# Kernel tuning notes

Measured on AMD Instinct MI355X. Metric: run time of the kernel, lower is better.

Reference implementation:

```python
import jax, jax.numpy as jnp
import numpy as np

NUM_SELECT = 300

def _cxcywh_to_xyxy(b):
    cx, cy, w, h = b[..., 0], b[..., 1], b[..., 2], b[..., 3]
    return jnp.stack([cx - w * 0.5, cy - h * 0.5, cx + w * 0.5, cy + h * 0.5], axis=-1)

def setup_inputs() -> dict:
    key = jax.random.key(0)
    k1, k2, k3 = jax.random.split(key, 3)
    B, Q, C = 512, 900, 256
    pred_logits = jax.random.normal(k1, (B, Q, C), dtype=jnp.float32)
    pred_boxes = jax.random.uniform(k2, (B, Q, 4), dtype=jnp.float32)  # normalized cxcywh in [0,1)
    target_sizes = jax.random.uniform(k3, (B, 2), dtype=jnp.float32) * 1333.0 + 1.0  # (h, w)
    return {"pred_logits": pred_logits, "pred_boxes": pred_boxes, "target_sizes": target_sizes}

def reference(pred_logits, pred_boxes, target_sizes):
    B, Q, C = pred_logits.shape
    prob = jax.nn.sigmoid(pred_logits)                      # [B,Q,C]
    flat = prob.reshape(B, Q * C)
    topk_vals, topk_idxs = jax.lax.top_k(flat, NUM_SELECT)  # [B,K]
    scores = topk_vals
    topk_boxes = topk_idxs // C                              # query index
    labels = topk_idxs % C                                   # class index
    out_boxes = _cxcywh_to_xyxy(pred_boxes)                  # [B,Q,4]
    out_boxes = jnp.take_along_axis(out_boxes, topk_boxes[:, :, None], axis=1)  # [B,K,4]
    img_h, img_w = target_sizes[:, 0], target_sizes[:, 1]
    scale = jnp.stack([img_w, img_h, img_w, img_h], axis=1)  # [B,4]
    out_boxes = out_boxes * scale[:, None, :]
    return scores, labels, out_boxes
```

## Files before the change

kernel.cpp:

```cpp
#include <hip/hip_runtime.h>
#include <math.h>


#define NB 512
#define NQ 900
#define NC 256
#define NELEM (NQ*NC)
#define NF4 (NELEM/4)
#define NSEL 300
#define NT 1024
#define HBINS 8192
#define CAP 2048

typedef unsigned long long ull;

__device__ __forceinline__ unsigned keyOf(float f) {
    unsigned u = __float_as_uint(f);
    return u ^ ((unsigned)((int)u >> 31) | 0x80000000u);
}
__device__ __forceinline__ float keyToFloat(unsigned k) {
    unsigned u = (k & 0x80000000u) ? (k ^ 0x80000000u) : ~k;
    return __uint_as_float(u);
}

__global__ __launch_bounds__(NT) void detpost_kernel(
    const float* __restrict__ logits, const float* __restrict__ boxes,
    const float* __restrict__ tsizes, float* __restrict__ out)
{
    __shared__ unsigned hist[HBINS];
    __shared__ ull zb[CAP];
    __shared__ unsigned suf[NT];
    __shared__ unsigned sT, sCand, sAbove, sDone, sCnt;

    const int tid = threadIdx.x;
    const int row = blockIdx.x;
    const float4* __restrict__ r4 = (const float4*)(logits + (size_t)row * NELEM);

    unsigned W0 = 0;
    unsigned sh = 19;
    unsigned above = 0;
    unsigned T, cand;

    while (true) {
        for (int i = tid; i < HBINS; i += NT) hist[i] = 0;
        __syncthreads();

        unsigned i0 = tid;
        #pragma unroll 1
        for (int it = 0; it < 14; ++it, i0 += 4096) {
            float4 a = r4[i0];
            float4 b = r4[i0 + 1024];
            float4 c = r4[i0 + 2048];
            float4 d = r4[i0 + 3072];
            #define PH(f) { unsigned k = keyOf(f); unsigned bin = (k - W0) >> sh; \
                            if (bin < HBINS) atomicAdd(&hist[bin], 1u); }
            PH(a.x) PH(a.y) PH(a.z) PH(a.w)
            PH(b.x) PH(b.y) PH(b.z) PH(b.w)
            PH(c.x) PH(c.y) PH(c.z) PH(c.w)
            PH(d.x) PH(d.y) PH(d.z) PH(d.w)
        }
        if (tid < 256) {
            float4 a = r4[57344 + tid];
            PH(a.x) PH(a.y) PH(a.z) PH(a.w)
        }
        __syncthreads();

        unsigned local = 0;
        #pragma unroll
        for (int j = 0; j < 8; ++j) local += hist[tid * 8 + j];
        suf[tid] = local;
        __syncthreads();
        for (int off = 1; off < NT; off <<= 1) {
            unsigned v = suf[tid] + ((tid + off < NT) ? suf[tid + off] : 0u);
            __syncthreads();
            suf[tid] = v;
            __syncthreads();
        }
        unsigned mySuf = suf[tid];
        unsigned nxt = (tid < NT - 1) ? suf[tid + 1] : 0u;
        if (above + mySuf >= NSEL && above + nxt < NSEL) {
            unsigned run = above + nxt;
            for (int j = 7; j >= 0; --j) {
                unsigned h = hist[tid * 8 + j];
                run += h;
                if (run >= NSEL) {
                    sT = W0 + ((unsigned)(tid * 8 + j) << sh);
                    sCand = run;
                    sAbove = run - h;
                    sDone = (run <= CAP || sh == 0) ? 1u : 0u;
                    break;
                }
            }
        }
        __syncthreads();
        T = sT; cand = sCand;
        if (sDone) break;
        above = sAbove;
        W0 = T;
        sh = (sh >= 13) ? (sh - 13) : 0u;
        __syncthreads();
    }
    (void)cand;

    if (tid == 0) sCnt = 0;
    __syncthreads();
    {
        unsigned i0 = tid;
        #pragma unroll 1
        for (int it = 0; it < 14; ++it, i0 += 4096) {
            float4 a = r4[i0];
            float4 b = r4[i0 + 1024];
            float4 c = r4[i0 + 2048];
            float4 d = r4[i0 + 3072];
            #define PC(f, ei) { unsigned k = keyOf(f); if (k >= T) { \
                unsigned p = atomicAdd(&sCnt, 1u); \
                if (p < CAP) zb[p] = ((ull)k << 32) | (unsigned)~(unsigned)(ei); } }
            PC(a.x, i0*4+0)          PC(a.y, i0*4+1)          PC(a.z, i0*4+2)          PC(a.w, i0*4+3)
            PC(b.x, (i0+1024)*4+0)   PC(b.y, (i0+1024)*4+1)   PC(b.z, (i0+1024)*4+2)   PC(b.w, (i0+1024)*4+3)
            PC(c.x, (i0+2048)*4+0)   PC(c.y, (i0+2048)*4+1)   PC(c.z, (i0+2048)*4+2)   PC(c.w, (i0+2048)*4+3)
            PC(d.x, (i0+3072)*4+0)   PC(d.y, (i0+3072)*4+1)   PC(d.z, (i0+3072)*4+2)   PC(d.w, (i0+3072)*4+3)
        }
        if (tid < 256) {
            float4 a = r4[57344 + tid];
            unsigned e0 = (57344 + tid) * 4;
            PC(a.x, e0+0) PC(a.y, e0+1) PC(a.z, e0+2) PC(a.w, e0+3)
        }
    }
    __syncthreads();
    unsigned cnt = min(sCnt, (unsigned)CAP);

    unsigned nSort = (cnt <= 1024u) ? 1024u : (unsigned)CAP;
    for (unsigned i = tid; i < nSort; i += NT)
        if (i >= cnt) zb[i] = 0ULL;
    __syncthreads();
    for (unsigned kk = 2; kk <= nSort; kk <<= 1) {
        for (unsigned j = kk >> 1; j > 0; j >>= 1) {
            for (unsigned i = tid; i < nSort; i += NT) {
                unsigned ixj = i ^ j;
                if (ixj > i) {
                    ull A = zb[i], B = zb[ixj];
                    bool sw = ((i & kk) == 0) ? (A < B) : (A > B);
                    if (sw) { zb[i] = B; zb[ixj] = A; }
                }
            }
            __syncthreads();
        }
    }

    if (tid < NSEL) {
        ull z = zb[tid];
        unsigned k   = (unsigned)(z >> 32);
        unsigned idx = ~(unsigned)z;
        float f = keyToFloat(k);
        double pd = 1.0 / (1.0 + exp(-(double)f));
        unsigned label = idx & (NC - 1);
        unsigned q = idx >> 8;
        float4 bx = ((const float4*)boxes)[(size_t)row * NQ + q];
        float imh = tsizes[row * 2 + 0];
        float imw = tsizes[row * 2 + 1];
        float x0 = (bx.x - bx.z * 0.5f) * imw;
        float y0 = (bx.y - bx.w * 0.5f) * imh;
        float x1 = (bx.x + bx.z * 0.5f) * imw;
        float y1 = (bx.y + bx.w * 0.5f) * imh;
        out[(size_t)row * NSEL + tid] = (float)pd;
        out[(size_t)NB * NSEL + (size_t)row * NSEL + tid] = (float)label;
        float* ob = out + (size_t)2 * NB * NSEL + ((size_t)row * NSEL + tid) * 4;
        ob[0] = x0; ob[1] = y0; ob[2] = x1; ob[3] = y1;
    }
}

extern "C" void kernel_launch(void* const* d_in, const int* in_sizes, int n_in,
                              void* d_out, int out_size, void* d_ws, size_t ws_size,
                              hipStream_t stream) {
    const float* logits = (const float*)d_in[0];
    const float* boxes  = (const float*)d_in[1];
    const float* tsz    = (const float*)d_in[2];
    float* out = (float*)d_out;
    detpost_kernel<<<NB, NT, 0, stream>>>(logits, boxes, tsz, out);
}
```

Baseline: 690.4 us.

## Keep per-thread top-6 in registers during one pass, radix-select on candidates

Replaces the multi-pass histogram radix select, which reread the 230K-element row once per refinement level plus once more for collection, with a single streaming pass. In that pass each thread keeps its top-6 keys in registers, and the radix select, compaction and bitonic sort then run only on those ~6K candidates. A fallback rescans the full row if any thread's 6th-best key could still fall inside the true top-300, which preserves exactness. The risk is extra register pressure and branching in the insertion step. Box output stores are also vectorised to float4.

```diff
diff --git a/kernel.cpp b/kernel.cpp
--- a/kernel.cpp
+++ b/kernel.cpp
@@ -9,7 +9,7 @@
 #define NF4 (NELEM/4)
 #define NSEL 300
 #define NT 1024
-#define HBINS 8192
+#define HB 4096
 #define CAP 2048
 
 typedef unsigned long long ull;
@@ -23,116 +23,7 @@
     return __uint_as_float(u);
 }
 
-__global__ __launch_bounds__(NT) void detpost_kernel(
-    const float* __restrict__ logits, const float* __restrict__ boxes,
-    const float* __restrict__ tsizes, float* __restrict__ out)
-{
-    __shared__ unsigned hist[HBINS];
-    __shared__ ull zb[CAP];
-    __shared__ unsigned suf[NT];
-    __shared__ unsigned sT, sCand, sAbove, sDone, sCnt;
-
-    const int tid = threadIdx.x;
-    const int row = blockIdx.x;
-    const float4* __restrict__ r4 = (const float4*)(logits + (size_t)row * NELEM);
-
-    unsigned W0 = 0;
-    unsigned sh = 19;
-    unsigned above = 0;
-    unsigned T, cand;
-
-    while (true) {
-        for (int i = tid; i < HBINS; i += NT) hist[i] = 0;
-        __syncthreads();
-
-        unsigned i0 = tid;
-        #pragma unroll 1
-        for (int it = 0; it < 14; ++it, i0 += 4096) {
-            float4 a = r4[i0];
-            float4 b = r4[i0 + 1024];
-            float4 c = r4[i0 + 2048];
-            float4 d = r4[i0 + 3072];
-            #define PH(f) { unsigned k = keyOf(f); unsigned bin = (k - W0) >> sh; \
-                            if (bin < HBINS) atomicAdd(&hist[bin], 1u); }
-            PH(a.x) PH(a.y) PH(a.z) PH(a.w)
-            PH(b.x) PH(b.y) PH(b.z) PH(b.w)
-            PH(c.x) PH(c.y) PH(c.z) PH(c.w)
-            PH(d.x) PH(d.y) PH(d.z) PH(d.w)
-        }
-        if (tid < 256) {
-            float4 a = r4[57344 + tid];
-            PH(a.x) PH(a.y) PH(a.z) PH(a.w)
-        }
-        __syncthreads();
-
-        unsigned local = 0;
-        #pragma unroll
-        for (int j = 0; j < 8; ++j) local += hist[tid * 8 + j];
-        suf[tid] = local;
-        __syncthreads();
-        for (int off = 1; off < NT; off <<= 1) {
-            unsigned v = suf[tid] + ((tid + off < NT) ? suf[tid + off] : 0u);
-            __syncthreads();
-            suf[tid] = v;
-            __syncthreads();
-        }
-        unsigned mySuf = suf[tid];
-        unsigned nxt = (tid < NT - 1) ? suf[tid + 1] : 0u;
-        if (above + mySuf >= NSEL && above + nxt < NSEL) {
-            unsigned run = above + nxt;
-            for (int j = 7; j >= 0; --j) {
-                unsigned h = hist[tid * 8 + j];
-                run += h;
-                if (run >= NSEL) {
-                    sT = W0 + ((unsigned)(tid * 8 + j) << sh);
-                    sCand = run;
-                    sAbove = run - h;
-                    sDone = (run <= CAP || sh == 0) ? 1u : 0u;
-                    break;
-                }
-            }
-        }
-        __syncthreads();
-        T = sT; cand = sCand;
-        if (sDone) break;
-        above = sAbove;
-        W0 = T;
-        sh = (sh >= 13) ? (sh - 13) : 0u;
-        __syncthreads();
-    }
-    (void)cand;
-
-    if (tid == 0) sCnt = 0;
-    __syncthreads();
-    {
-        unsigned i0 = tid;
-        #pragma unroll 1
-        for (int it = 0; it < 14; ++it, i0 += 4096) {
-            float4 a = r4[i0];
-            float4 b = r4[i0 + 1024];
-            float4 c = r4[i0 + 2048];
-            float4 d = r4[i0 + 3072];
-            #define PC(f, ei) { unsigned k = keyOf(f); if (k >= T) { \
-                unsigned p = atomicAdd(&sCnt, 1u); \
-                if (p < CAP) zb[p] = ((ull)k << 32) | (unsigned)~(unsigned)(ei); } }
-            PC(a.x, i0*4+0)          PC(a.y, i0*4+1)          PC(a.z, i0*4+2)          PC(a.w, i0*4+3)
-            PC(b.x, (i0+1024)*4+0)   PC(b.y, (i0+1024)*4+1)   PC(b.z, (i0+1024)*4+2)   PC(b.w, (i0+1024)*4+3)
-            PC(c.x, (i0+2048)*4+0)   PC(c.y, (i0+2048)*4+1)   PC(c.z, (i0+2048)*4+2)   PC(c.w, (i0+2048)*4+3)
-            PC(d.x, (i0+3072)*4+0)   PC(d.y, (i0+3072)*4+1)   PC(d.z, (i0+3072)*4+2)   PC(d.w, (i0+3072)*4+3)
-        }
-        if (tid < 256) {
-            float4 a = r4[57344 + tid];
-            unsigned e0 = (57344 + tid) * 4;
-            PC(a.x, e0+0) PC(a.y, e0+1) PC(a.z, e0+2) PC(a.w, e0+3)
-        }
-    }
-    __syncthreads();
-    unsigned cnt = min(sCnt, (unsigned)CAP);
-
-    unsigned nSort = (cnt <= 1024u) ? 1024u : (unsigned)CAP;
-    for (unsigned i = tid; i < nSort; i += NT)
-        if (i >= cnt) zb[i] = 0ULL;
-    __syncthreads();
+__device__ __forceinline__ void bitonicSortDesc(ull* zb, unsigned nSort, int tid) {
     for (unsigned kk = 2; kk <= nSort; kk <<= 1) {
         for (unsigned j = kk >> 1; j > 0; j >>= 1) {
             for (unsigned i = tid; i < nSort; i += NT) {
@@ -145,6 +36,149 @@
             }
             __syncthreads();
         }
+    }
+}
+
+__global__ __launch_bounds__(NT) void detpost_kernel(
+    const float* __restrict__ logits, const float* __restrict__ boxes,
+    const float* __restrict__ tsizes, float* __restrict__ out)
+{
+    __shared__ unsigned hist[HB];
+    __shared__ ull zb[CAP];
+    __shared__ unsigned suf[NT];
+    __shared__ unsigned sT, sCand, sAbove, sCnt, sFlag;
+
+    const int tid = threadIdx.x;
+    const int row = blockIdx.x;
+    const float4* __restrict__ r4 = (const float4*)(logits + (size_t)row * NELEM);
+
+    ull z0 = 0, z1 = 0, z2 = 0, z3 = 0, z4 = 0, z5 = 0;
+    unsigned key5 = 0;
+
+    #define INS(f, ei) { unsigned k = keyOf(f); if (k > key5) { \
+        ull z = ((ull)k << 32) | (unsigned)~(unsigned)(ei); \
+        if (z > z0)      { z5=z4; z4=z3; z3=z2; z2=z1; z1=z0; z0=z; } \
+        else if (z > z1) { z5=z4; z4=z3; z3=z2; z2=z1; z1=z; } \
+        else if (z > z2) { z5=z4; z4=z3; z3=z2; z2=z; } \
+        else if (z > z3) { z5=z4; z4=z3; z3=z; } \
+        else if (z > z4) { z5=z4; z4=z; } \
+        else             { z5=z; } \
+        key5 = (unsigned)(z5 >> 32); } }
+
+    {
+        unsigned i0 = tid;
+        #pragma unroll 1
+        for (int it = 0; it < 14; ++it, i0 += 4096) {
+            float4 a = r4[i0];
+            float4 b = r4[i0 + 1024];
+            float4 c = r4[i0 + 2048];
+            float4 d = r4[i0 + 3072];
+            unsigned e = i0 * 4u;
+            INS(a.x, e)         INS(a.y, e+1)       INS(a.z, e+2)       INS(a.w, e+3)
+            INS(b.x, e+4096)    INS(b.y, e+4097)    INS(b.z, e+4098)    INS(b.w, e+4099)
+            INS(c.x, e+8192)    INS(c.y, e+8193)    INS(c.z, e+8194)    INS(c.w, e+8195)
+            INS(d.x, e+12288)   INS(d.y, e+12289)   INS(d.z, e+12290)   INS(d.w, e+12291)
+        }
+        if (tid < 256) {
+            float4 a = r4[57344 + tid];
+            unsigned e = (57344u + tid) * 4u;
+            INS(a.x, e) INS(a.y, e+1) INS(a.z, e+2) INS(a.w, e+3)
+        }
+    }
+
+    unsigned T, cand;
+    unsigned W0 = 0; int sh = 20; int wlog2 = 32;
+    while (true) {
+        for (int i = tid; i < HB; i += NT) hist[i] = 0;
+        if (tid == 0) sAbove = 0;
+        __syncthreads();
+
+        const ull wtop = (wlog2 >= 32) ? (1ULL << 32) : ((ull)W0 + (1ULL << wlog2));
+        #define HZ(zz) { unsigned k = (unsigned)((zz) >> 32); if (k >= W0) { \
+            if ((ull)k < wtop) atomicAdd(&hist[(k - W0) >> sh], 1u); \
+            else atomicAdd(&sAbove, 1u); } }
+        HZ(z0) HZ(z1) HZ(z2) HZ(z3) HZ(z4) HZ(z5)
+        #undef HZ
+        __syncthreads();
+
+        unsigned local = 0;
+        #pragma unroll
+        for (int j = 0; j < 4; ++j) local += hist[tid * 4 + j];
+        suf[tid] = local;
+        __syncthreads();
+        for (int off = 1; off < NT; off <<= 1) {
+            unsigned v = suf[tid] + ((tid + off < NT) ? suf[tid + off] : 0u);
+            __syncthreads();
+            suf[tid] = v;
+            __syncthreads();
+        }
+        const unsigned above = sAbove;
+        const unsigned mySuf = suf[tid];
+        const unsigned nxt = (tid < NT - 1) ? suf[tid + 1] : 0u;
+        if (above + mySuf >= NSEL && above + nxt < NSEL) {
+            unsigned run = above + nxt;
+            for (int j = 3; j >= 0; --j) {
+                run += hist[tid * 4 + j];
+                if (run >= NSEL) {
+                    sT = W0 + ((unsigned)(tid * 4 + j) << sh);
+                    sCand = run;
+                    break;
+                }
+            }
+        }
+        __syncthreads();
+        T = sT; cand = sCand;
+        if (cand <= 512 || sh == 0) break;
+        W0 = T; wlog2 = sh; sh = (sh > 12) ? (sh - 12) : 0;
+    }
+
+    if (tid == 0) { sCnt = 0; sFlag = 0; }
+    __syncthreads();
+    #define APP(zz) { if ((unsigned)((zz) >> 32) >= T) { \
+        unsigned p = atomicAdd(&sCnt, 1u); if (p < CAP) zb[p] = (zz); } }
+    APP(z0) APP(z1) APP(z2) APP(z3) APP(z4) APP(z5)
+    #undef APP
+    __syncthreads();
+    unsigned cnt = min(sCnt, (unsigned)CAP);
+    unsigned nSort = (cnt <= 512u) ? 512u : (cnt <= 1024u ? 1024u : (unsigned)CAP);
+    for (unsigned i = tid; i < nSort; i += NT) if (i >= cnt) zb[i] = 0ULL;
+    __syncthreads();
+    bitonicSortDesc(zb, nSort, tid);
+
+    const unsigned Khat = (unsigned)(zb[NSEL - 1] >> 32);
+    if (key5 > Khat) sFlag = 1u;
+    __syncthreads();
+    if (sFlag) {
+        if (tid == 0) sCnt = 0;
+        __syncthreads();
+        #define PC(f, ei) { unsigned k = keyOf(f); if (k >= Khat) { \
+            unsigned p = atomicAdd(&sCnt, 1u); \
+            if (p < CAP) zb[p] = ((ull)k << 32) | (unsigned)~(unsigned)(ei); } }
+        unsigned i0 = tid;
+        #pragma unroll 1
+        for (int it = 0; it < 14; ++it, i0 += 4096) {
+            float4 a = r4[i0];
+            float4 b = r4[i0 + 1024];
+            float4 c = r4[i0 + 2048];
+            float4 d = r4[i0 + 3072];
+            unsigned e = i0 * 4u;
+            PC(a.x, e)         PC(a.y, e+1)       PC(a.z, e+2)       PC(a.w, e+3)
+            PC(b.x, e+4096)    PC(b.y, e+4097)    PC(b.z, e+4098)    PC(b.w, e+4099)
+            PC(c.x, e+8192)    PC(c.y, e+8193)    PC(c.z, e+8194)    PC(c.w, e+8195)
+            PC(d.x, e+12288)   PC(d.y, e+12289)   PC(d.z, e+12290)   PC(d.w, e+12291)
+        }
+        if (tid < 256) {
+            float4 a = r4[57344 + tid];
+            unsigned e = (57344u + tid) * 4u;
+            PC(a.x, e) PC(a.y, e+1) PC(a.z, e+2) PC(a.w, e+3)
+        }
+        #undef PC
+        __syncthreads();
+        cnt = min(sCnt, (unsigned)CAP);
+        nSort = (cnt <= 512u) ? 512u : (cnt <= 1024u ? 1024u : (unsigned)CAP);
+        for (unsigned i = tid; i < nSort; i += NT) if (i >= cnt) zb[i] = 0ULL;
+        __syncthreads();
+        bitonicSortDesc(zb, nSort, tid);
     }
 
     if (tid < NSEL) {
@@ -164,8 +198,8 @@
         float y1 = (bx.y + bx.w * 0.5f) * imh;
         out[(size_t)row * NSEL + tid] = (float)pd;
         out[(size_t)NB * NSEL + (size_t)row * NSEL + tid] = (float)label;
-        float* ob = out + (size_t)2 * NB * NSEL + ((size_t)row * NSEL + tid) * 4;
-        ob[0] = x0; ob[1] = y0; ob[2] = x1; ob[3] = y1;
+        float4* ob = (float4*)(out + (size_t)2 * NB * NSEL + ((size_t)row * NSEL + tid) * 4);
+        *ob = make_float4(x0, y0, x1, y1);
     }
 }
 
```

New measurement: 654.0 us. 5.3% less time.
